# Performance work log

Measured on AMD Instinct MI355X. Metric: run time of the kernel, lower is better.

## Reference

```python
import jax, jax.numpy as jnp
import numpy as np

EMB_DIM = 1024
N_HEADS = 16
HEAD_DIM = EMB_DIM // N_HEADS


def setup_inputs() -> dict:
    key = jax.random.key(0)
    ks = jax.random.split(key, 6)
    B, S, D = 2, 2048, EMB_DIM
    scale = 1.0 / np.sqrt(D)
    return {
        "in_data": jax.random.normal(ks[0], (B, S, D), dtype=jnp.float32),
        "Wq": jax.random.normal(ks[1], (D, D), dtype=jnp.float32) * scale,
        "Wk": jax.random.normal(ks[2], (D, D), dtype=jnp.float32) * scale,
        "Wv": jax.random.normal(ks[3], (D, D), dtype=jnp.float32) * scale,
        "Wo": jax.random.normal(ks[4], (D, D), dtype=jnp.float32) * scale,
        "bo": jax.random.normal(ks[5], (D,), dtype=jnp.float32) * 0.01,
    }


def reference(in_data, Wq, Wk, Wv, Wo, bo):
    B, S, D = in_data.shape
    H, Hd = N_HEADS, HEAD_DIM
    # Linear projections (qvbias=False): torch Linear is x @ W.T
    q = in_data @ Wq.T
    k = in_data @ Wk.T
    v = in_data @ Wv.T
    # split heads -> (B, H, S, Hd)
    q = q.reshape(B, S, H, Hd).transpose(0, 2, 1, 3)
    k = k.reshape(B, S, H, Hd).transpose(0, 2, 1, 3)
    v = v.reshape(B, S, H, Hd).transpose(0, 2, 1, 3)
    # scores (B, H, S, S), causal mask applied BEFORE scaling (as in source)
    scores = jnp.einsum("bhqd,bhkd->bhqk", q, k)
    causal = jnp.triu(jnp.ones((S, S), dtype=bool), k=1)
    scores = jnp.where(causal, -jnp.inf, scores)
    scores = scores / jnp.sqrt(jnp.asarray(Hd, dtype=scores.dtype))
    attn = jax.nn.softmax(scores, axis=-1)
    # dropout with drop_rate=0.0 -> identity
    ctx = jnp.einsum("bhqk,bhkd->bhqd", attn, v)
    ctx = ctx.transpose(0, 2, 1, 3).reshape(B, S, D)
    out = ctx @ Wo.T + bo
    return out
```

## Files before the change

### kernel.cpp

```cpp
#include <hip/hip_runtime.h>

typedef _Float16 f16;
typedef _Float16 f16x4 __attribute__((ext_vector_type(4)));
typedef _Float16 f16x8 __attribute__((ext_vector_type(8)));
typedef float f32x4 __attribute__((ext_vector_type(4)));

#define MFMA(a, b, c) __builtin_amdgcn_mfma_f32_16x16x32_f16((a), (b), (c), 0, 0, 0)

typedef __attribute__((address_space(1))) const void gvoid;
typedef __attribute__((address_space(3))) void lvoid;

__device__ __forceinline__ void gload16(const void* g, void* l) {
    __builtin_amdgcn_global_load_lds((gvoid*)g, (lvoid*)l, 16, 0, 0);
}

__global__ void cast_all(const float* __restrict__ x,
                         const float* __restrict__ w0, const float* __restrict__ w1,
                         const float* __restrict__ w2, const float* __restrict__ w3,
                         f16* __restrict__ xb, f16* __restrict__ wb) {
    const int NX = 4096 * 1024;
    int i = (blockIdx.x * 256 + threadIdx.x) * 4;
    if (i < NX) {
        float4 v = *(const float4*)(x + i);
        f16x4 o = {(f16)v.x, (f16)v.y, (f16)v.z, (f16)v.w};
        *(f16x4*)(xb + i) = o;
    } else {
        int j = i - NX;
        const float* s = (j < (1 << 20)) ? w0 : (j < (2 << 20)) ? w1
                       : (j < (3 << 20)) ? w2 : w3;
        int loc = j & ((1 << 20) - 1);
        float4 v = *(const float4*)(s + loc);
        f16x4 o = {(f16)v.x, (f16)v.y, (f16)v.z, (f16)v.w};
        *(f16x4*)(wb + j) = o;
    }
}

template <bool FINAL>
__global__ void gemm_bt(const f16* __restrict__ A, const f16* __restrict__ Bw,
                        f16* __restrict__ Cf, f16* __restrict__ VTo,
                        float* __restrict__ Co, const float* __restrict__ bias) {
    __shared__ __align__(16) f16 As[128 * 64];
    __shared__ __align__(16) f16 Bs[128 * 64];
    const int tid = threadIdx.x;
    const int lane = tid & 63, wid = tid >> 6;
    const int lo = lane & 15, hi = lane >> 4;
    const int wr = wid >> 1, wc = wid & 1;
    const int m0 = blockIdx.x * 128, n0 = blockIdx.y * 128;
    const char* Ab = (const char*)A;
    const char* Bb = (const char*)(Bw + (size_t)blockIdx.z * (1024 * 1024));

    f32x4 acc[4][4];
#pragma unroll
    for (int i = 0; i < 4; ++i)
#pragma unroll
        for (int j = 0; j < 4; ++j) acc[i][j] = (f32x4){0.f, 0.f, 0.f, 0.f};

    for (int kt = 0; kt < 16; ++kt) {
        const int kb = kt * 128;
#pragma unroll
        for (int rr = 0; rr < 4; ++rr) {
            int o = rr * 4096 + tid * 16;
            int row = o >> 7, colB = o & 127;
            gload16(Ab + (size_t)(m0 + row) * 2048 + kb + colB, (char*)As + o);
            gload16(Bb + (size_t)(n0 + row) * 2048 + kb + colB, (char*)Bs + o);
        }
        __syncthreads();
#pragma unroll
        for (int kc = 0; kc < 2; ++kc) {
            f16x8 af[4], bf[4];
#pragma unroll
            for (int f = 0; f < 4; ++f)
                af[f] = *(const f16x8*)(As + (wr * 64 + f * 16 + lo) * 64 + kc * 32 + hi * 8);
#pragma unroll
            for (int f = 0; f < 4; ++f)
                bf[f] = *(const f16x8*)(Bs + (wc * 64 + f * 16 + lo) * 64 + kc * 32 + hi * 8);
#pragma unroll
            for (int i = 0; i < 4; ++i)
#pragma unroll
                for (int j = 0; j < 4; ++j) acc[i][j] = MFMA(af[i], bf[j], acc[i][j]);
        }
        __syncthreads();
    }

    const int mbase = m0 + wr * 64 + hi * 4;
    const int nbase = n0 + wc * 64 + lo;
    if (FINAL) {
#pragma unroll
        for (int j = 0; j < 4; ++j) {
            float bj = bias[nbase + j * 16];
#pragma unroll
            for (int i = 0; i < 4; ++i)
#pragma unroll
                for (int r = 0; r < 4; ++r)
                    Co[(size_t)(mbase + i * 16 + r) * 1024 + nbase + j * 16] =
                        acc[i][j][r] + bj;
        }
    } else if (blockIdx.z == 2) {
#pragma unroll
        for (int i = 0; i < 4; ++i)
#pragma unroll
            for (int j = 0; j < 4; ++j)
#pragma unroll
                for (int r = 0; r < 4; ++r) {
                    int m = mbase + i * 16 + r, n = nbase + j * 16;
                    VTo[(size_t)((m >> 11) * 1024 + n) * 2048 + (m & 2047)] =
                        (f16)acc[i][j][r];
                }
    } else {
        const float osc = (blockIdx.z == 0) ? 0.125f : 1.0f;
        f16* Cz = Cf + (size_t)blockIdx.z * (4096 * 1024);
#pragma unroll
        for (int i = 0; i < 4; ++i)
#pragma unroll
            for (int j = 0; j < 4; ++j)
#pragma unroll
                for (int r = 0; r < 4; ++r)
                    Cz[(size_t)(mbase + i * 16 + r) * 1024 + nbase + j * 16] =
                        (f16)(acc[i][j][r] * osc);
    }
}

__global__ __launch_bounds__(256) void attn(const f16* __restrict__ Q,
                                            const f16* __restrict__ K,
                                            const f16* __restrict__ VT,
                                            f16* __restrict__ CTX) {
    __shared__ __align__(16) f16 K0[64 * 64];
    __shared__ __align__(16) f16 K1[64 * 64];
    __shared__ __align__(16) f16 V0[64 * 64];
    __shared__ __align__(16) f16 V1[64 * 64];
    __shared__ __align__(16) f16 Pl[4 * 16 * 72];
    const int tid = threadIdx.x;
    const int lane = tid & 63, w = tid >> 6;
    const int lo = lane & 15, hi = lane >> 4;
    const int bh = blockIdx.x;
    const int qt = 31 - blockIdx.y;
    const int b = bh >> 4, h = bh & 15;
    const int qw0 = qt * 64 + w * 16;
    const int qglob = qw0 + lo;

    const f16* qrow = Q + (size_t)(b * 2048 + qw0 + lo) * 1024 + h * 64 + hi * 8;
    const f16x8 qa0 = *(const f16x8*)(qrow);
    const f16x8 qa1 = *(const f16x8*)(qrow + 32);

    f32x4 ctx[4];
#pragma unroll
    for (int d = 0; d < 4; ++d) ctx[d] = (f32x4){0.f, 0.f, 0.f, 0.f};
    float mrun = -3e38f, lrun = 0.f;

    f16* Pw = Pl + w * (16 * 72);
    const char* Kb = (const char*)K;
    const char* Vb = (const char*)VT;

    auto stage = [&](f16* Kd, f16* Vd, int t) {
        const int kv0 = t * 64;
#pragma unroll
        for (int rr = 0; rr < 2; ++rr) {
            int o = rr * 4096 + tid * 16;
            int row = o >> 7;
            int colB = (o & 127) ^ ((row & 7) << 4);
            gload16(Kb + (size_t)(b * 2048 + kv0 + row) * 2048 + h * 128 + colB,
                    (char*)Kd + o);
            gload16(Vb + (size_t)(b * 1024 + h * 64 + row) * 4096 + (size_t)kv0 * 2 + colB,
                    (char*)Vd + o);
        }
    };

    auto compute = [&](const f16* Klb, const f16* Vlb, int t) {
        f32x4 s4[4];
        __builtin_amdgcn_s_setprio(1);
#pragma unroll
        for (int fj = 0; fj < 4; ++fj) {
            f32x4 a = (f32x4){0.f, 0.f, 0.f, 0.f};
            const int kv = fj * 16 + lo;
#pragma unroll
            for (int kc = 0; kc < 2; ++kc) {
                const int cb = (kc * 64 + hi * 16) ^ ((kv & 7) << 4);
                f16x8 kf = *(const f16x8*)((const char*)Klb + kv * 128 + cb);
                a = MFMA(kf, kc ? qa1 : qa0, a);
            }
            s4[fj] = a;
        }
        __builtin_amdgcn_s_setprio(0);

        float pv[16];
        if (t == qt) {
#pragma unroll
            for (int fj = 0; fj < 4; ++fj)
#pragma unroll
                for (int r = 0; r < 4; ++r) {
                    const int kvg = t * 64 + fj * 16 + hi * 4 + r;
                    pv[fj * 4 + r] = (kvg > qglob) ? -3e38f : s4[fj][r];
                }
        } else {
#pragma unroll
            for (int fj = 0; fj < 4; ++fj)
#pragma unroll
                for (int r = 0; r < 4; ++r) pv[fj * 4 + r] = s4[fj][r];
        }

        float tm[8];
#pragma unroll
        for (int i = 0; i < 8; ++i) tm[i] = fmaxf(pv[i], pv[i + 8]);
#pragma unroll
        for (int i = 0; i < 4; ++i) tm[i] = fmaxf(tm[i], tm[i + 4]);
        float mx = fmaxf(fmaxf(tm[0], tm[1]), fmaxf(tm[2], tm[3]));
        mx = fmaxf(mx, __shfl_xor(mx, 16));
        mx = fmaxf(mx, __shfl_xor(mx, 32));

        const float mnew = fmaxf(mrun, mx);
        const float corr = __expf(mrun - mnew);
        mrun = mnew;
#pragma unroll
        for (int i = 0; i < 16; ++i) pv[i] = __expf(pv[i] - mnew);
        float ts[8];
#pragma unroll
        for (int i = 0; i < 8; ++i) ts[i] = pv[i] + pv[i + 8];
#pragma unroll
        for (int i = 0; i < 4; ++i) ts[i] = ts[i] + ts[i + 4];
        float rs = (ts[0] + ts[1]) + (ts[2] + ts[3]);
        rs += __shfl_xor(rs, 16);
        rs += __shfl_xor(rs, 32);
        lrun = lrun * corr + rs;

#pragma unroll
        for (int r = 0; r < 4; ++r) {
            const float cq = __shfl(corr, hi * 4 + r);
            ctx[0][r] *= cq; ctx[1][r] *= cq; ctx[2][r] *= cq; ctx[3][r] *= cq;
        }

#pragma unroll
        for (int fj = 0; fj < 4; ++fj) {
            f16x4 w4 = {(f16)pv[fj * 4 + 0], (f16)pv[fj * 4 + 1],
                        (f16)pv[fj * 4 + 2], (f16)pv[fj * 4 + 3]};
            *(f16x4*)(Pw + lo * 72 + fj * 16 + hi * 4) = w4;
        }
        const f16x8 pa0 = *(const f16x8*)(Pw + lo * 72 + hi * 8);
        const f16x8 pa1 = *(const f16x8*)(Pw + lo * 72 + 32 + hi * 8);

        __builtin_amdgcn_s_setprio(1);
#pragma unroll
        for (int df = 0; df < 4; ++df) {
            const int d = df * 16 + lo;
#pragma unroll
            for (int kc = 0; kc < 2; ++kc) {
                const int cb = (kc * 64 + hi * 16) ^ ((d & 7) << 4);
                f16x8 vf = *(const f16x8*)((const char*)Vlb + d * 128 + cb);
                ctx[df] = MFMA(kc ? pa1 : pa0, vf, ctx[df]);
            }
        }
        __builtin_amdgcn_s_setprio(0);
    };

    stage(&K0[0], &V0[0], 0);
    for (int t = 0; t <= qt; ++t) {
        __syncthreads();
        if ((t & 1) == 0) {
            if (t < qt) stage(&K1[0], &V1[0], t + 1);
            compute(&K0[0], &V0[0], t);
        } else {
            if (t < qt) stage(&K0[0], &V0[0], t + 1);
            compute(&K1[0], &V1[0], t);
        }
    }

#pragma unroll
    for (int r = 0; r < 4; ++r) {
        const float lq = __shfl(lrun, hi * 4 + r);
        const float inv = 1.0f / lq;
#pragma unroll
        for (int df = 0; df < 4; ++df)
            CTX[(size_t)(b * 2048 + qw0 + hi * 4 + r) * 1024 + h * 64 + df * 16 + lo] =
                (f16)(ctx[df][r] * inv);
    }
}

extern "C" void kernel_launch(void* const* d_in, const int* in_sizes, int n_in,
                              void* d_out, int out_size, void* d_ws, size_t ws_size,
                              hipStream_t stream) {
    const float* x = (const float*)d_in[0];
    const float* wq = (const float*)d_in[1];
    const float* wk = (const float*)d_in[2];
    const float* wv = (const float*)d_in[3];
    const float* wo = (const float*)d_in[4];
    const float* bo = (const float*)d_in[5];

    const size_t M1 = 1024 * 1024;
    f16* VT = (f16*)d_ws;
    f16* Wh = VT + 4 * M1;
    f16* QKV = Wh + 4 * M1;
    f16* Xb = QKV + 8 * M1;
    f16* Q = QKV;
    f16* K = QKV + 4 * M1;
    f16* CTX = QKV + 8 * M1;
    float* out = (float*)d_out;

    cast_all<<<dim3(8192), dim3(256), 0, stream>>>(x, wq, wk, wv, wo, Xb, Wh);
    gemm_bt<false><<<dim3(32, 8, 3), dim3(256), 0, stream>>>(Xb, Wh, QKV, VT, nullptr, nullptr);
    attn<<<dim3(32, 32), dim3(256), 0, stream>>>(Q, K, VT, CTX);
    gemm_bt<true><<<dim3(32, 8, 1), dim3(256), 0, stream>>>(CTX, Wh + 3 * M1, nullptr, nullptr, out, bo);
}
```

Measured before the change: 185.5 us.

## Rework attention softmax: exp2 prescale, lazy rescale, register-shuffle P operand

Folds log2(e) into the Q scale so the softmax uses exp2 directly. The running max is only updated when a row max grows by more than 8, which skips most rescaling and max shuffles, and row sums are reduced once at the end. The P tile is passed to the PV MFMA through lane shuffles instead of an LDS round trip, with the operands swapped so the output is transposed and written as vectorized stores. This risks overflow or precision loss if the deferred max lags too far.

```diff
diff --git a/kernel.cpp b/kernel.cpp
--- a/kernel.cpp
+++ b/kernel.cpp
@@ -1,9 +1,11 @@
 #include <hip/hip_runtime.h>
 
 typedef _Float16 f16;
+typedef _Float16 f16x2 __attribute__((ext_vector_type(2)));
 typedef _Float16 f16x4 __attribute__((ext_vector_type(4)));
 typedef _Float16 f16x8 __attribute__((ext_vector_type(8)));
 typedef float f32x4 __attribute__((ext_vector_type(4)));
+typedef int i32x4 __attribute__((ext_vector_type(4)));
 
 #define MFMA(a, b, c) __builtin_amdgcn_mfma_f32_16x16x32_f16((a), (b), (c), 0, 0, 0)
 
@@ -107,7 +109,7 @@
                         (f16)acc[i][j][r];
                 }
     } else {
-        const float osc = (blockIdx.z == 0) ? 0.125f : 1.0f;
+        const float osc = (blockIdx.z == 0) ? 0.18033688f : 1.0f;
         f16* Cz = Cf + (size_t)blockIdx.z * (4096 * 1024);
 #pragma unroll
         for (int i = 0; i < 4; ++i)
@@ -128,7 +130,6 @@
     __shared__ __align__(16) f16 K1[64 * 64];
     __shared__ __align__(16) f16 V0[64 * 64];
     __shared__ __align__(16) f16 V1[64 * 64];
-    __shared__ __align__(16) f16 Pl[4 * 16 * 72];
     const int tid = threadIdx.x;
     const int lane = tid & 63, w = tid >> 6;
     const int lo = lane & 15, hi = lane >> 4;
@@ -145,9 +146,11 @@
     f32x4 ctx[4];
 #pragma unroll
     for (int d = 0; d < 4; ++d) ctx[d] = (f32x4){0.f, 0.f, 0.f, 0.f};
-    float mrun = -3e38f, lrun = 0.f;
-
-    f16* Pw = Pl + w * (16 * 72);
+    float mrun = -3e38f, lsum = 0.f;
+
+    const int idx0 = (2 * (hi & 1)) * 16 + lo;
+    const int idx1 = idx0 + 16;
+
     const char* Kb = (const char*)K;
     const char* Vb = (const char*)VT;
 
@@ -189,7 +192,7 @@
 #pragma unroll
                 for (int r = 0; r < 4; ++r) {
                     const int kvg = t * 64 + fj * 16 + hi * 4 + r;
-                    pv[fj * 4 + r] = (kvg > qglob) ? -3e38f : s4[fj][r];
+                    pv[fj * 4 + r] = (kvg > qglob) ? -1e38f : s4[fj][r];
                 }
         } else {
 #pragma unroll
@@ -203,39 +206,53 @@
         for (int i = 0; i < 8; ++i) tm[i] = fmaxf(pv[i], pv[i + 8]);
 #pragma unroll
         for (int i = 0; i < 4; ++i) tm[i] = fmaxf(tm[i], tm[i + 4]);
-        float mx = fmaxf(fmaxf(tm[0], tm[1]), fmaxf(tm[2], tm[3]));
-        mx = fmaxf(mx, __shfl_xor(mx, 16));
-        mx = fmaxf(mx, __shfl_xor(mx, 32));
-
-        const float mnew = fmaxf(mrun, mx);
-        const float corr = __expf(mrun - mnew);
-        mrun = mnew;
-#pragma unroll
-        for (int i = 0; i < 16; ++i) pv[i] = __expf(pv[i] - mnew);
+        const float mxl = fmaxf(fmaxf(tm[0], tm[1]), fmaxf(tm[2], tm[3]));
+
+        if (__any(mxl > mrun + 8.0f)) {
+            float mxg = fmaxf(mxl, __shfl_xor(mxl, 16));
+            mxg = fmaxf(mxg, __shfl_xor(mxg, 32));
+            const float mnew = fmaxf(mrun, mxg);
+            const float corr = __builtin_amdgcn_exp2f(mrun - mnew);
+            mrun = mnew;
+            lsum *= corr;
+#pragma unroll
+            for (int d = 0; d < 4; ++d) {
+                ctx[d][0] *= corr; ctx[d][1] *= corr;
+                ctx[d][2] *= corr; ctx[d][3] *= corr;
+            }
+        }
+
+#pragma unroll
+        for (int i = 0; i < 16; ++i) pv[i] = __builtin_amdgcn_exp2f(pv[i] - mrun);
         float ts[8];
 #pragma unroll
         for (int i = 0; i < 8; ++i) ts[i] = pv[i] + pv[i + 8];
 #pragma unroll
         for (int i = 0; i < 4; ++i) ts[i] = ts[i] + ts[i + 4];
-        float rs = (ts[0] + ts[1]) + (ts[2] + ts[3]);
-        rs += __shfl_xor(rs, 16);
-        rs += __shfl_xor(rs, 32);
-        lrun = lrun * corr + rs;
-
-#pragma unroll
-        for (int r = 0; r < 4; ++r) {
-            const float cq = __shfl(corr, hi * 4 + r);
-            ctx[0][r] *= cq; ctx[1][r] *= cq; ctx[2][r] *= cq; ctx[3][r] *= cq;
-        }
-
-#pragma unroll
-        for (int fj = 0; fj < 4; ++fj) {
-            f16x4 w4 = {(f16)pv[fj * 4 + 0], (f16)pv[fj * 4 + 1],
-                        (f16)pv[fj * 4 + 2], (f16)pv[fj * 4 + 3]};
-            *(f16x4*)(Pw + lo * 72 + fj * 16 + hi * 4) = w4;
-        }
-        const f16x8 pa0 = *(const f16x8*)(Pw + lo * 72 + hi * 8);
-        const f16x8 pa1 = *(const f16x8*)(Pw + lo * 72 + 32 + hi * 8);
+        lsum += (ts[0] + ts[1]) + (ts[2] + ts[3]);
+
+        int ph[4][2];
+#pragma unroll
+        for (int fj = 0; fj < 4; ++fj)
+#pragma unroll
+            for (int r2 = 0; r2 < 2; ++r2) {
+                f16x2 hpair = {(f16)pv[fj * 4 + 2 * r2], (f16)pv[fj * 4 + 2 * r2 + 1]};
+                ph[fj][r2] = __builtin_bit_cast(int, hpair);
+            }
+
+        f16x8 pb[2];
+#pragma unroll
+        for (int kc = 0; kc < 2; ++kc) {
+            i32x4 dw;
+#pragma unroll
+            for (int j2 = 0; j2 < 4; ++j2) {
+                const int idx = (j2 < 2) ? idx0 : idx1;
+                int vA = __shfl(ph[2 * kc][j2 & 1], idx);
+                int vB = __shfl(ph[2 * kc + 1][j2 & 1], idx);
+                dw[j2] = (hi & 2) ? vB : vA;
+            }
+            pb[kc] = __builtin_bit_cast(f16x8, dw);
+        }
 
         __builtin_amdgcn_s_setprio(1);
 #pragma unroll
@@ -245,7 +262,7 @@
             for (int kc = 0; kc < 2; ++kc) {
                 const int cb = (kc * 64 + hi * 16) ^ ((d & 7) << 4);
                 f16x8 vf = *(const f16x8*)((const char*)Vlb + d * 128 + cb);
-                ctx[df] = MFMA(kc ? pa1 : pa0, vf, ctx[df]);
+                ctx[df] = MFMA(vf, pb[kc], ctx[df]);
             }
         }
         __builtin_amdgcn_s_setprio(0);
@@ -263,14 +280,14 @@
         }
     }
 
-#pragma unroll
-    for (int r = 0; r < 4; ++r) {
-        const float lq = __shfl(lrun, hi * 4 + r);
-        const float inv = 1.0f / lq;
-#pragma unroll
-        for (int df = 0; df < 4; ++df)
-            CTX[(size_t)(b * 2048 + qw0 + hi * 4 + r) * 1024 + h * 64 + df * 16 + lo] =
-                (f16)(ctx[df][r] * inv);
+    float lt = lsum + __shfl_xor(lsum, 16);
+    lt += __shfl_xor(lt, 32);
+    const float inv = 1.0f / lt;
+#pragma unroll
+    for (int df = 0; df < 4; ++df) {
+        f16x4 o = {(f16)(ctx[df][0] * inv), (f16)(ctx[df][1] * inv),
+                   (f16)(ctx[df][2] * inv), (f16)(ctx[df][3] * inv)};
+        *(f16x4*)(CTX + (size_t)(b * 2048 + qw0 + lo) * 1024 + h * 64 + df * 16 + hi * 4) = o;
     }
 }
 
```

New measurement: 185.9 us. No clear change (+0.2%).
